# Kernel optimization log

Hardware: AMD Instinct MI355X
Metric: run time of the kernel (lower is better)

Reference implementation:

```python
import jax, jax.numpy as jnp
import numpy as np

E, D_IN, D_OUT = 8, 1024, 1024
B, S = 4, 2048

def setup_inputs() -> dict:
    key = jax.random.key(0)
    k_x, k_g, k_gb, k_w = jax.random.split(key, 4)
    x = jax.random.normal(k_x, (B, S, D_IN), dtype=jnp.float32)
    gate_w = jax.random.normal(k_g, (D_IN, E), dtype=jnp.float32) * 0.02
    gate_b = jax.random.normal(k_gb, (E,), dtype=jnp.float32) * 0.02
    expert_w = jax.random.normal(k_w, (E, D_IN, D_OUT), dtype=jnp.float32) * 0.02
    return {"x": x, "gate_w": gate_w, "gate_b": gate_b, "expert_w": expert_w}

def reference(x, gate_w, gate_b, expert_w):
    # gate: softmax over experts
    gate_score = jax.nn.softmax(x @ gate_w + gate_b, axis=-1)        # [B,S,E]
    # all-expert dense GEMM: [B,S,E,out]
    expert_out = jnp.einsum('bsi,eio->bseo', x, expert_w)
    # gate-weighted combine: [B,S,out]
    out = jnp.einsum('bse,bseo->bso', gate_score, expert_out)
    return out
```

## Files before the change

kernel.cpp:

```cpp
#include <hip/hip_runtime.h>
#include <hip/hip_bf16.h>
#include <cstdint>

#define TOKENS 8192
#define DIN 1024
#define DOUT 1024
#define NE 8

typedef __bf16 bf16;
typedef __attribute__((ext_vector_type(8))) __bf16 bf16x8;
typedef __attribute__((ext_vector_type(4))) float floatx4;
typedef __attribute__((ext_vector_type(2))) float floatx2;

__device__ __forceinline__ void async16(const void* gptr, void* lptr) {
  __builtin_amdgcn_global_load_lds(
      (const __attribute__((address_space(1))) void*)gptr,
      (__attribute__((address_space(3))) void*)lptr,
      16, 0, 0);
}

__global__ __launch_bounds__(256) void gate_kernel(
    const float* __restrict__ x, const float* __restrict__ gw,
    const float* __restrict__ gb, float* __restrict__ g,
    bf16* __restrict__ xb) {
  const int lane = threadIdx.x & 63;
  const int wave = threadIdx.x >> 6;
  const int t = blockIdx.x * 4 + wave;
  const float* xr = x + (size_t)t * DIN;
  bf16* xbr = xb + (size_t)t * DIN;

  float acc[NE];
#pragma unroll
  for (int e = 0; e < NE; ++e) acc[e] = 0.f;

#pragma unroll
  for (int it = 0; it < 8; ++it) {
    const int i = it * 128 + lane * 2;
    const floatx2 xv = *(const floatx2*)(xr + i);
    union { bf16 b[2]; uint32_t u; } cv;
    cv.b[0] = (bf16)xv[0]; cv.b[1] = (bf16)xv[1];
    *(uint32_t*)(xbr + i) = cv.u;
    const floatx4 w00 = *(const floatx4*)(gw + (size_t)i * NE);
    const floatx4 w01 = *(const floatx4*)(gw + (size_t)i * NE + 4);
    const floatx4 w10 = *(const floatx4*)(gw + (size_t)(i + 1) * NE);
    const floatx4 w11 = *(const floatx4*)(gw + (size_t)(i + 1) * NE + 4);
#pragma unroll
    for (int e = 0; e < 4; ++e) {
      acc[e]     += xv[0] * w00[e] + xv[1] * w10[e];
      acc[e + 4] += xv[0] * w01[e] + xv[1] * w11[e];
    }
  }
#pragma unroll
  for (int e = 0; e < NE; ++e) {
#pragma unroll
    for (int off = 32; off > 0; off >>= 1)
      acc[e] += __shfl_xor(acc[e], off, 64);
  }
  float lg[NE];
  float mx = -3.0e38f;
#pragma unroll
  for (int e = 0; e < NE; ++e) { lg[e] = acc[e] + gb[e]; mx = fmaxf(mx, lg[e]); }
  float s = 0.f;
#pragma unroll
  for (int e = 0; e < NE; ++e) { lg[e] = __expf(lg[e] - mx); s += lg[e]; }
  const float inv = 1.f / s;
  if (lane == 0) {
    floatx4 o0, o1;
#pragma unroll
    for (int e = 0; e < 4; ++e) { o0[e] = lg[e] * inv; o1[e] = lg[e + 4] * inv; }
    *(floatx4*)(g + (size_t)t * NE) = o0;
    *(floatx4*)(g + (size_t)t * NE + 4) = o1;
  }
}

__global__ __launch_bounds__(256) void wt_kernel(
    const float* __restrict__ w, bf16* __restrict__ wt) {
  __shared__ float tile[64][65];
  const int e = blockIdx.z;
  const int i0 = blockIdx.y * 64;
  const int o0 = blockIdx.x * 64;
  const int tid = threadIdx.x;
  const int c4 = (tid & 15) * 4;
  const int r = tid >> 4;

  const float* src = w + ((size_t)e * DIN + i0) * DOUT + o0;
#pragma unroll
  for (int rr = r; rr < 64; rr += 16) {
    const floatx4 v = *(const floatx4*)(src + (size_t)rr * DOUT + c4);
    tile[rr][c4] = v[0]; tile[rr][c4 + 1] = v[1];
    tile[rr][c4 + 2] = v[2]; tile[rr][c4 + 3] = v[3];
  }
  __syncthreads();
  bf16* dst = wt + ((size_t)e * DOUT + o0) * DIN + i0;
#pragma unroll
  for (int rr = r; rr < 64; rr += 16) {
    union { bf16 b[4]; uint64_t u; } cv;
#pragma unroll
    for (int j = 0; j < 4; ++j) cv.b[j] = (bf16)tile[c4 + j][rr];
    *(uint64_t*)(dst + (size_t)rr * DIN + c4) = cv.u;
  }
}

__global__ __launch_bounds__(256, 2) void moe_gemm(
    const bf16* __restrict__ xb, const bf16* __restrict__ wt,
    const float* __restrict__ g, float* __restrict__ out) {
  __shared__ __align__(16) bf16 As[128 * 32];
  __shared__ __align__(16) bf16 Bs[128 * 32];

  const int tid = threadIdx.x;
  const int bm = blockIdx.x >> 3;
  const int bn = blockIdx.x & 7;
  const int lane = tid & 63;
  const int wave = tid >> 6;
  const int wm = wave >> 1, wn = wave & 1;
  const int lr = lane & 15, lq = lane >> 4;

  const int srow = tid >> 2;
  const int scol = (((tid & 3) ^ ((tid >> 3) & 3)) << 3);

  const bf16* agp = xb + ((size_t)(bm * 128 + srow)) * DIN + scol;
  bf16* const alp = As + tid * 8;
  bf16* const blp = Bs + tid * 8;

  const int kgp = ((lq ^ ((lr >> 1) & 3)) << 3);

  const floatx4 fzero = {0.f, 0.f, 0.f, 0.f};
  floatx4 accF[4][4];
#pragma unroll
  for (int im = 0; im < 4; ++im)
#pragma unroll
    for (int in = 0; in < 4; ++in) accF[im][in] = fzero;

  const int tok0 = bm * 128 + wm * 64;

  for (int e = 0; e < NE; ++e) {
    const bf16* bgp = wt + ((size_t)e << 20) +
                      ((size_t)(bn * 128 + srow)) * DIN + scol;
    floatx4 accE[4][4];
#pragma unroll
    for (int im = 0; im < 4; ++im)
#pragma unroll
      for (int in = 0; in < 4; ++in) accE[im][in] = fzero;

    for (int k0 = 0; k0 < DIN; k0 += 32) {
      __syncthreads();
      async16(agp + k0, alp);
      async16(agp + (size_t)64 * DIN + k0, alp + 2048);
      async16(bgp + k0, blp);
      async16(bgp + (size_t)64 * DIN + k0, blp + 2048);
      __syncthreads();

      bf16x8 av[4], bv[4];
#pragma unroll
      for (int im = 0; im < 4; ++im)
        av[im] = *(const bf16x8*)(As + (wm * 64 + im * 16 + lr) * 32 + kgp);
#pragma unroll
      for (int in = 0; in < 4; ++in)
        bv[in] = *(const bf16x8*)(Bs + (wn * 64 + in * 16 + lr) * 32 + kgp);
#pragma unroll
      for (int im = 0; im < 4; ++im)
#pragma unroll
        for (int in = 0; in < 4; ++in)
          accE[im][in] = __builtin_amdgcn_mfma_f32_16x16x32_bf16(
              av[im], bv[in], accE[im][in], 0, 0, 0);
    }

#pragma unroll
    for (int im = 0; im < 4; ++im) {
      float gv[4];
#pragma unroll
      for (int r = 0; r < 4; ++r)
        gv[r] = g[(size_t)(tok0 + im * 16 + lq * 4 + r) * NE + e];
#pragma unroll
      for (int in = 0; in < 4; ++in)
#pragma unroll
        for (int r = 0; r < 4; ++r)
          accF[im][in][r] += gv[r] * accE[im][in][r];
    }
  }

#pragma unroll
  for (int im = 0; im < 4; ++im)
#pragma unroll
    for (int in = 0; in < 4; ++in) {
      const int col = bn * 128 + wn * 64 + in * 16 + lr;
#pragma unroll
      for (int r = 0; r < 4; ++r)
        out[(size_t)(tok0 + im * 16 + lq * 4 + r) * DOUT + col] =
            accF[im][in][r];
    }
}

extern "C" void kernel_launch(void* const* d_in, const int* in_sizes, int n_in,
                              void* d_out, int out_size, void* d_ws,
                              size_t ws_size, hipStream_t stream) {
  const float* x  = (const float*)d_in[0];
  const float* gw = (const float*)d_in[1];
  const float* gb = (const float*)d_in[2];
  const float* w  = (const float*)d_in[3];
  float* out = (float*)d_out;

  char* ws = (char*)d_ws;
  float* g  = (float*)ws;
  bf16* xb  = (bf16*)(ws + 262144);
  bf16* wt  = (bf16*)(ws + 262144 + (size_t)TOKENS * DIN * 2);

  gate_kernel<<<TOKENS / 4, 256, 0, stream>>>(x, gw, gb, g, xb);
  dim3 wtg(DOUT / 64, DIN / 64, NE);
  wt_kernel<<<wtg, 256, 0, stream>>>(w, wt);
  moe_gemm<<<512, 256, 0, stream>>>(xb, wt, g, out);
}
```

Measured before the change: 284.1 us.

## Merge gate and weight-transpose kernels; double GEMM K-tile to 64 with wider swizzle

The gate/bf16-cast kernel and the weight transpose kernel become one launch that dispatches on block index, which removes one launch and lets the two memory-bound jobs overlap. The GEMM K step grows from 32 to 64, so each stage loads 128x64 tiles with an 8-way XOR swizzle and runs two MFMA sub-steps per barrier pair. This halves the number of __syncthreads per expert, at the cost of twice the LDS (32 KB per block), which may limit occupancy.

```diff
diff --git a/kernel.cpp b/kernel.cpp
--- a/kernel.cpp
+++ b/kernel.cpp
@@ -19,93 +19,95 @@
       16, 0, 0);
 }
 
-__global__ __launch_bounds__(256) void gate_kernel(
+__global__ __launch_bounds__(256) void prep_kernel(
     const float* __restrict__ x, const float* __restrict__ gw,
     const float* __restrict__ gb, float* __restrict__ g,
-    bf16* __restrict__ xb) {
-  const int lane = threadIdx.x & 63;
-  const int wave = threadIdx.x >> 6;
-  const int t = blockIdx.x * 4 + wave;
-  const float* xr = x + (size_t)t * DIN;
-  bf16* xbr = xb + (size_t)t * DIN;
-
-  float acc[NE];
-#pragma unroll
-  for (int e = 0; e < NE; ++e) acc[e] = 0.f;
-
-#pragma unroll
-  for (int it = 0; it < 8; ++it) {
-    const int i = it * 128 + lane * 2;
-    const floatx2 xv = *(const floatx2*)(xr + i);
-    union { bf16 b[2]; uint32_t u; } cv;
-    cv.b[0] = (bf16)xv[0]; cv.b[1] = (bf16)xv[1];
-    *(uint32_t*)(xbr + i) = cv.u;
-    const floatx4 w00 = *(const floatx4*)(gw + (size_t)i * NE);
-    const floatx4 w01 = *(const floatx4*)(gw + (size_t)i * NE + 4);
-    const floatx4 w10 = *(const floatx4*)(gw + (size_t)(i + 1) * NE);
-    const floatx4 w11 = *(const floatx4*)(gw + (size_t)(i + 1) * NE + 4);
-#pragma unroll
-    for (int e = 0; e < 4; ++e) {
-      acc[e]     += xv[0] * w00[e] + xv[1] * w10[e];
-      acc[e + 4] += xv[0] * w01[e] + xv[1] * w11[e];
-    }
-  }
-#pragma unroll
-  for (int e = 0; e < NE; ++e) {
-#pragma unroll
-    for (int off = 32; off > 0; off >>= 1)
-      acc[e] += __shfl_xor(acc[e], off, 64);
-  }
-  float lg[NE];
-  float mx = -3.0e38f;
-#pragma unroll
-  for (int e = 0; e < NE; ++e) { lg[e] = acc[e] + gb[e]; mx = fmaxf(mx, lg[e]); }
-  float s = 0.f;
-#pragma unroll
-  for (int e = 0; e < NE; ++e) { lg[e] = __expf(lg[e] - mx); s += lg[e]; }
-  const float inv = 1.f / s;
-  if (lane == 0) {
-    floatx4 o0, o1;
-#pragma unroll
-    for (int e = 0; e < 4; ++e) { o0[e] = lg[e] * inv; o1[e] = lg[e + 4] * inv; }
-    *(floatx4*)(g + (size_t)t * NE) = o0;
-    *(floatx4*)(g + (size_t)t * NE + 4) = o1;
-  }
-}
-
-__global__ __launch_bounds__(256) void wt_kernel(
-    const float* __restrict__ w, bf16* __restrict__ wt) {
+    bf16* __restrict__ xb, const float* __restrict__ w,
+    bf16* __restrict__ wt) {
   __shared__ float tile[64][65];
-  const int e = blockIdx.z;
-  const int i0 = blockIdx.y * 64;
-  const int o0 = blockIdx.x * 64;
-  const int tid = threadIdx.x;
-  const int c4 = (tid & 15) * 4;
-  const int r = tid >> 4;
-
-  const float* src = w + ((size_t)e * DIN + i0) * DOUT + o0;
-#pragma unroll
-  for (int rr = r; rr < 64; rr += 16) {
-    const floatx4 v = *(const floatx4*)(src + (size_t)rr * DOUT + c4);
-    tile[rr][c4] = v[0]; tile[rr][c4 + 1] = v[1];
-    tile[rr][c4 + 2] = v[2]; tile[rr][c4 + 3] = v[3];
-  }
-  __syncthreads();
-  bf16* dst = wt + ((size_t)e * DOUT + o0) * DIN + i0;
-#pragma unroll
-  for (int rr = r; rr < 64; rr += 16) {
-    union { bf16 b[4]; uint64_t u; } cv;
-#pragma unroll
-    for (int j = 0; j < 4; ++j) cv.b[j] = (bf16)tile[c4 + j][rr];
-    *(uint64_t*)(dst + (size_t)rr * DIN + c4) = cv.u;
+
+  if (blockIdx.x < 2048) {
+    const int lane = threadIdx.x & 63;
+    const int wave = threadIdx.x >> 6;
+    const int t = blockIdx.x * 4 + wave;
+    const float* xr = x + (size_t)t * DIN;
+    bf16* xbr = xb + (size_t)t * DIN;
+
+    float acc[NE];
+#pragma unroll
+    for (int e = 0; e < NE; ++e) acc[e] = 0.f;
+
+#pragma unroll
+    for (int it = 0; it < 8; ++it) {
+      const int i = it * 128 + lane * 2;
+      const floatx2 xv = *(const floatx2*)(xr + i);
+      union { bf16 b[2]; uint32_t u; } cv;
+      cv.b[0] = (bf16)xv[0]; cv.b[1] = (bf16)xv[1];
+      *(uint32_t*)(xbr + i) = cv.u;
+      const floatx4 w00 = *(const floatx4*)(gw + (size_t)i * NE);
+      const floatx4 w01 = *(const floatx4*)(gw + (size_t)i * NE + 4);
+      const floatx4 w10 = *(const floatx4*)(gw + (size_t)(i + 1) * NE);
+      const floatx4 w11 = *(const floatx4*)(gw + (size_t)(i + 1) * NE + 4);
+#pragma unroll
+      for (int e = 0; e < 4; ++e) {
+        acc[e]     += xv[0] * w00[e] + xv[1] * w10[e];
+        acc[e + 4] += xv[0] * w01[e] + xv[1] * w11[e];
+      }
+    }
+#pragma unroll
+    for (int e = 0; e < NE; ++e) {
+#pragma unroll
+      for (int off = 32; off > 0; off >>= 1)
+        acc[e] += __shfl_xor(acc[e], off, 64);
+    }
+    float lg[NE];
+    float mx = -3.0e38f;
+#pragma unroll
+    for (int e = 0; e < NE; ++e) { lg[e] = acc[e] + gb[e]; mx = fmaxf(mx, lg[e]); }
+    float s = 0.f;
+#pragma unroll
+    for (int e = 0; e < NE; ++e) { lg[e] = __expf(lg[e] - mx); s += lg[e]; }
+    const float inv = 1.f / s;
+    if (lane == 0) {
+      floatx4 o0, o1;
+#pragma unroll
+      for (int e = 0; e < 4; ++e) { o0[e] = lg[e] * inv; o1[e] = lg[e + 4] * inv; }
+      *(floatx4*)(g + (size_t)t * NE) = o0;
+      *(floatx4*)(g + (size_t)t * NE + 4) = o1;
+    }
+  } else {
+    const int b = blockIdx.x - 2048;
+    const int e = b >> 8;
+    const int i0 = ((b >> 4) & 15) * 64;
+    const int o0 = (b & 15) * 64;
+    const int tid = threadIdx.x;
+    const int c4 = (tid & 15) * 4;
+    const int r = tid >> 4;
+
+    const float* src = w + ((size_t)e * DIN + i0) * DOUT + o0;
+#pragma unroll
+    for (int rr = r; rr < 64; rr += 16) {
+      const floatx4 v = *(const floatx4*)(src + (size_t)rr * DOUT + c4);
+      tile[rr][c4] = v[0]; tile[rr][c4 + 1] = v[1];
+      tile[rr][c4 + 2] = v[2]; tile[rr][c4 + 3] = v[3];
+    }
+    __syncthreads();
+    bf16* dst = wt + ((size_t)e * DOUT + o0) * DIN + i0;
+#pragma unroll
+    for (int rr = r; rr < 64; rr += 16) {
+      union { bf16 b[4]; uint64_t u; } cv;
+#pragma unroll
+      for (int j = 0; j < 4; ++j) cv.b[j] = (bf16)tile[c4 + j][rr];
+      *(uint64_t*)(dst + (size_t)rr * DIN + c4) = cv.u;
+    }
   }
 }
 
 __global__ __launch_bounds__(256, 2) void moe_gemm(
     const bf16* __restrict__ xb, const bf16* __restrict__ wt,
     const float* __restrict__ g, float* __restrict__ out) {
-  __shared__ __align__(16) bf16 As[128 * 32];
-  __shared__ __align__(16) bf16 Bs[128 * 32];
+  __shared__ __align__(16) bf16 As[128 * 64];
+  __shared__ __align__(16) bf16 Bs[128 * 64];
 
   const int tid = threadIdx.x;
   const int bm = blockIdx.x >> 3;
@@ -115,14 +117,14 @@
   const int wm = wave >> 1, wn = wave & 1;
   const int lr = lane & 15, lq = lane >> 4;
 
-  const int srow = tid >> 2;
-  const int scol = (((tid & 3) ^ ((tid >> 3) & 3)) << 3);
+  const int srow = tid >> 3;
+  const int scol = (((tid & 7) ^ (srow & 7)) << 3);
 
   const bf16* agp = xb + ((size_t)(bm * 128 + srow)) * DIN + scol;
   bf16* const alp = As + tid * 8;
   bf16* const blp = Bs + tid * 8;
 
-  const int kgp = ((lq ^ ((lr >> 1) & 3)) << 3);
+  const int kx = lr & 7;
 
   const floatx4 fzero = {0.f, 0.f, 0.f, 0.f};
   floatx4 accF[4][4];
@@ -142,27 +144,32 @@
 #pragma unroll
       for (int in = 0; in < 4; ++in) accE[im][in] = fzero;
 
-    for (int k0 = 0; k0 < DIN; k0 += 32) {
+    for (int k0 = 0; k0 < DIN; k0 += 64) {
       __syncthreads();
-      async16(agp + k0, alp);
-      async16(agp + (size_t)64 * DIN + k0, alp + 2048);
-      async16(bgp + k0, blp);
-      async16(bgp + (size_t)64 * DIN + k0, blp + 2048);
+#pragma unroll
+      for (int j = 0; j < 4; ++j) {
+        async16(agp + k0 + (size_t)(32 * j) * DIN, alp + j * 2048);
+        async16(bgp + k0 + (size_t)(32 * j) * DIN, blp + j * 2048);
+      }
       __syncthreads();
 
-      bf16x8 av[4], bv[4];
-#pragma unroll
-      for (int im = 0; im < 4; ++im)
-        av[im] = *(const bf16x8*)(As + (wm * 64 + im * 16 + lr) * 32 + kgp);
-#pragma unroll
-      for (int in = 0; in < 4; ++in)
-        bv[in] = *(const bf16x8*)(Bs + (wn * 64 + in * 16 + lr) * 32 + kgp);
-#pragma unroll
-      for (int im = 0; im < 4; ++im)
+#pragma unroll
+      for (int h = 0; h < 2; ++h) {
+        const int kg = ((h * 4 + lq) ^ kx) << 3;
+        bf16x8 av[4], bv[4];
+#pragma unroll
+        for (int im = 0; im < 4; ++im)
+          av[im] = *(const bf16x8*)(As + (wm * 64 + im * 16 + lr) * 64 + kg);
 #pragma unroll
         for (int in = 0; in < 4; ++in)
-          accE[im][in] = __builtin_amdgcn_mfma_f32_16x16x32_bf16(
-              av[im], bv[in], accE[im][in], 0, 0, 0);
+          bv[in] = *(const bf16x8*)(Bs + (wn * 64 + in * 16 + lr) * 64 + kg);
+#pragma unroll
+        for (int im = 0; im < 4; ++im)
+#pragma unroll
+          for (int in = 0; in < 4; ++in)
+            accE[im][in] = __builtin_amdgcn_mfma_f32_16x16x32_bf16(
+                av[im], bv[in], accE[im][in], 0, 0, 0);
+      }
     }
 
 #pragma unroll
@@ -205,8 +212,6 @@
   bf16* xb  = (bf16*)(ws + 262144);
   bf16* wt  = (bf16*)(ws + 262144 + (size_t)TOKENS * DIN * 2);
 
-  gate_kernel<<<TOKENS / 4, 256, 0, stream>>>(x, gw, gb, g, xb);
-  dim3 wtg(DOUT / 64, DIN / 64, NE);
-  wt_kernel<<<wtg, 256, 0, stream>>>(w, wt);
+  prep_kernel<<<4096, 256, 0, stream>>>(x, gw, gb, g, xb, w, wt);
   moe_gemm<<<512, 256, 0, stream>>>(xb, wt, g, out);
 }
```

Measured after the change: 271.5 us. 1.05x faster.
